# Kernel tuning notes

Measured on AMD Instinct MI355X. Metric: run time of the kernel, lower is better.

## Reference

```python
import jax, jax.numpy as jnp
import numpy as np

NEGPOS_RATIO = 3


def _smooth_l1(pred, tgt):
    d = jnp.abs(pred - tgt)
    return jnp.where(d < 1.0, 0.5 * d * d, d - 0.5)


def setup_inputs() -> dict:
    key = jax.random.key(0)
    B, P, C = 64, 8732, 81
    ks = jax.random.split(key, 7)
    loc_dataT = jax.random.normal(ks[0], (B, P, 4), jnp.float32)
    conf_dataT = jax.random.normal(ks[1], (B, P, C), jnp.float32)
    loc_dataS = jax.random.normal(ks[2], (B, P, 4), jnp.float32)
    conf_dataS = jax.random.normal(ks[3], (B, P, C), jnp.float32)
    loc_t = jax.random.normal(ks[4], (B, P, 4), jnp.float32)
    is_pos = jax.random.uniform(ks[5], (B, P)) < 0.02
    labels = jax.random.randint(ks[6], (B, P), 1, C, dtype=jnp.int32)
    conf_t = jnp.where(is_pos, labels, 0).astype(jnp.int32)
    return {
        "loc_dataT": loc_dataT, "conf_dataT": conf_dataT,
        "loc_dataS": loc_dataS, "conf_dataS": conf_dataS,
        "loc_t": loc_t, "conf_t": conf_t,
    }


def _multibox_losses(loc_dataT, conf_dataT, loc_dataS, conf_dataS, loc_t, conf_t):
    B, P, C = conf_dataT.shape
    pos = conf_t > 0                                    # [B,P]
    posf = pos.astype(conf_dataT.dtype)

    # Localization SmoothL1 over positive priors (reduction='sum')
    loss_lT = jnp.sum(_smooth_l1(loc_dataT, loc_t) * posf[..., None])
    loss_lS = jnp.sum(_smooth_l1(loc_dataS, loc_t) * posf[..., None])

    # Per-prior CE loss: logsumexp(conf) - conf[gt]  (== -log_softmax[gt])
    def per_prior_ce(conf):
        lse = jax.nn.logsumexp(conf, axis=-1)           # [B,P]
        gt = jnp.take_along_axis(conf, conf_t[..., None].astype(jnp.int32), axis=-1)[..., 0]
        return lse - gt

    lcT = per_prior_ce(conf_dataT)                      # [B,P]
    lcS = per_prior_ce(conf_dataS)

    # Hard negative mining: rank negatives by loss (positives zeroed first)
    def neg_mask(lc, num_neg):
        lc_m = jnp.where(pos, 0.0, lc)
        order = jnp.argsort(-lc_m, axis=1)              # descending sort indices
        rank = jnp.argsort(order, axis=1)               # rank of each prior
        return rank < num_neg

    num_pos = jnp.sum(pos.astype(jnp.int32), axis=1, keepdims=True)   # [B,1]
    num_neg = jnp.minimum(NEGPOS_RATIO * num_pos, P - 1)
    negT = neg_mask(lcT, num_neg)
    negS = neg_mask(lcS, num_neg)

    # Confidence CE over positives + mined negatives (reduction='sum')
    loss_cT = jnp.sum(jnp.where(pos | negT, lcT, 0.0))
    loss_cS = jnp.sum(jnp.where(pos | negS, lcS, 0.0))

    N = jnp.sum(num_pos).astype(conf_dataT.dtype)
    return jnp.stack([loss_lT / N, loss_cT / N, loss_lS / N, loss_cS / N])


def reference(loc_dataT, conf_dataT, loc_dataS, conf_dataS, loc_t, conf_t):
    # Teacher branch is detached in the original module.
    loc_dataT = jax.lax.stop_gradient(loc_dataT)
    conf_dataT = jax.lax.stop_gradient(conf_dataT)
    return _multibox_losses(loc_dataT, conf_dataT, loc_dataS, conf_dataS, loc_t, conf_t)
```

## Files before the change

kernel.cpp:

```cpp
#include <hip/hip_runtime.h>
#include <hip/hip_bf16.h>

#define BB 64
#define PP 8732
#define CC 81
#define RPB 128


__device__ __forceinline__ float sl1(float d) {
    d = fabsf(d);
    return d < 1.0f ? 0.5f * d * d : d - 0.5f;
}

__device__ __forceinline__ float blockReduceF(float v, volatile float* sb) {
    for (int off = 32; off; off >>= 1) v += __shfl_xor(v, off, 64);
    __syncthreads();
    if ((threadIdx.x & 63) == 0) sb[threadIdx.x >> 6] = v;
    __syncthreads();
    float r = 0.0f;
    int nw = blockDim.x >> 6;
    for (int i = 0; i < nw; ++i) r += sb[i];
    return r;
}

__device__ __forceinline__ int blockReduceI(int v, volatile int* sb) {
    for (int off = 32; off; off >>= 1) v += __shfl_xor(v, off, 64);
    __syncthreads();
    if ((threadIdx.x & 63) == 0) sb[threadIdx.x >> 6] = v;
    __syncthreads();
    int r = 0;
    int nw = blockDim.x >> 6;
    for (int i = 0; i < nw; ++i) r += sb[i];
    return r;
}

__global__ void kInit(float* acc, int* numpos) {
    int t = threadIdx.x;
    if (t < 4) acc[t] = 0.0f;
    if (t < BB) numpos[t] = 0;
}

__global__ __launch_bounds__(1024) void kA(const float4* __restrict__ locT,
                                           const float4* __restrict__ locS,
                                           const float4* __restrict__ loct,
                                           const int* __restrict__ conft,
                                           float* acc, int* numpos) {
    __shared__ float fsb[16];
    __shared__ int isb[16];
    int b = blockIdx.y;
    int p = blockIdx.x * blockDim.x + threadIdx.x;
    float sT = 0.0f, sS = 0.0f;
    int cnt = 0;
    if (p < PP) {
        size_t i = (size_t)b * PP + p;
        int t = conft[i];
        if (t > 0) {
            cnt = 1;
            float4 g = loct[i];
            float4 aT = locT[i];
            float4 aS = locS[i];
            sT = sl1(aT.x - g.x) + sl1(aT.y - g.y) + sl1(aT.z - g.z) + sl1(aT.w - g.w);
            sS = sl1(aS.x - g.x) + sl1(aS.y - g.y) + sl1(aS.z - g.z) + sl1(aS.w - g.w);
        }
    }
    sT = blockReduceF(sT, fsb);
    sS = blockReduceF(sS, fsb);
    cnt = blockReduceI(cnt, isb);
    if (threadIdx.x == 0) {
        if (sT != 0.0f) atomicAdd(&acc[0], sT);
        if (sS != 0.0f) atomicAdd(&acc[1], sS);
        if (cnt) atomicAdd(&numpos[b], cnt);
    }
}

__global__ __launch_bounds__(256) void kB(const float* __restrict__ confT,
                                          const float* __restrict__ confS,
                                          const int* __restrict__ conft,
                                          float* __restrict__ lcT,
                                          float* __restrict__ lcS) {
    __shared__ float rowsum[RPB];
    __shared__ float gtval[RPB];
    __shared__ int gtofs[RPB];
    __shared__ int gtraw[RPB];
    int b = blockIdx.y;
    int p0 = blockIdx.x * RPB;
    int nrows = min(RPB, PP - p0);
    int tid = threadIdx.x;
    const float* __restrict__ conf = blockIdx.z ? confS : confT;
    float* __restrict__ dst = blockIdx.z ? lcS : lcT;
    size_t rowBase = (size_t)b * PP + p0;

    for (int r = tid; r < nrows; r += 256) {
        int g = conft[rowBase + r];
        gtraw[r] = g;
        gtofs[r] = r * CC + g;
        rowsum[r] = 0.0f;
        gtval[r] = 0.0f;
    }
    __syncthreads();

    const float4* __restrict__ g4 = (const float4*)(conf + rowBase * CC);
    int nq = (nrows * CC) >> 2;
    for (int i = tid; i < nq; i += 256) {
        float4 v = g4[i];
        int f = i << 2;
        int r0 = f / 81;
        int rem = f - r0 * 81;
        int r1 = (rem + 3 >= 81) ? r0 + 1 : r0;
        float e0 = __expf(v.x), e1 = __expf(v.y), e2 = __expf(v.z), e3 = __expf(v.w);
        float t01 = e0 + e1, t23 = e2 + e3, tot = t01 + t23;
        if (r1 == r0) {
            atomicAdd(&rowsum[r0], tot);
        } else {
            int nsplit = 81 - rem;
            float a = (nsplit == 1) ? e0 : ((nsplit == 2) ? t01 : t01 + e2);
            atomicAdd(&rowsum[r0], a);
            atomicAdd(&rowsum[r1], tot - a);
        }
        int j = gtofs[r0] - f;
        if (j >= 0 && j < 4) gtval[r0] = ((const float*)&v)[j];
        if (r1 != r0) {
            int j1 = gtofs[r1] - f;
            if (j1 >= 0 && j1 < 4) gtval[r1] = ((const float*)&v)[j1];
        }
    }
    __syncthreads();

    for (int r = tid; r < nrows; r += 256) {
        float lc = __logf(rowsum[r]) - gtval[r];
        dst[rowBase + r] = (gtraw[r] > 0) ? -(lc + 1.0f) : lc;
    }
}

__global__ __launch_bounds__(1024) void kC(const float* __restrict__ lcT,
                                           const float* __restrict__ lcS,
                                           const int* __restrict__ numpos,
                                           float* acc) {
    __shared__ unsigned keys[PP];
    __shared__ int hist[256];
    __shared__ float fsb[16];
    __shared__ int isb[16];
    __shared__ int selBin, selAbove;
    int b = blockIdx.y;
    int tid = threadIdx.x;
    const float* src = ((blockIdx.x == 0) ? lcT : lcS) + (size_t)b * PP;

    float posSum = 0.0f;
    for (int i = tid; i < PP; i += 1024) {
        float v = src[i];
        keys[i] = (v < 0.0f) ? 0u : __float_as_uint(v);
        if (v < 0.0f) posSum += (-v - 1.0f);
    }
    posSum = blockReduceF(posSum, fsb);

    int np = numpos[b];
    int k = min(3 * np, PP - 1);
    float mined = 0.0f;
    if (k > 0) {
        unsigned prefix = 0;
        int kk = k;
        for (int round = 0; round < 4; ++round) {
            int shift = 24 - 8 * round;
            if (tid < 256) hist[tid] = 0;
            __syncthreads();
            for (int i = tid; i < PP; i += 1024) {
                unsigned key = keys[i];
                bool match = (round == 0) || ((key >> (shift + 8)) == prefix);
                if (match) atomicAdd(&hist[(key >> shift) & 0xFF], 1);
            }
            __syncthreads();
            for (int d = 1; d < 256; d <<= 1) {
                int v2 = 0;
                if (tid < 256) v2 = hist[tid] + ((tid + d < 256) ? hist[tid + d] : 0);
                __syncthreads();
                if (tid < 256) hist[tid] = v2;
                __syncthreads();
            }
            if (tid < 256) {
                int above = (tid < 255) ? hist[tid + 1] : 0;
                if (above < kk && hist[tid] >= kk) {
                    selBin = tid;
                    selAbove = above;
                }
            }
            __syncthreads();
            prefix = (prefix << 8) | (unsigned)selBin;
            kk -= selAbove;
            __syncthreads();
        }
        int c = 0;
        float s = 0.0f;
        for (int i = tid; i < PP; i += 1024) {
            unsigned key = keys[i];
            if (key > prefix) { c += 1; s += __uint_as_float(key); }
        }
        c = blockReduceI(c, isb);
        s = blockReduceF(s, fsb);
        mined = s + (float)(k - c) * __uint_as_float(prefix);
    }
    if (tid == 0) atomicAdd(&acc[(blockIdx.x == 0) ? 2 : 3], posSum + mined);
}

__global__ void kD(const float* acc, const int* numpos, float* out) {
    int v = (threadIdx.x < BB) ? numpos[threadIdx.x] : 0;
    for (int off = 32; off; off >>= 1) v += __shfl_xor(v, off, 64);
    if (threadIdx.x == 0) {
        float N = (float)v;
        out[0] = acc[0] / N;
        out[1] = acc[2] / N;
        out[2] = acc[1] / N;
        out[3] = acc[3] / N;
    }
}

extern "C" void kernel_launch(void* const* d_in, const int* in_sizes, int n_in,
                              void* d_out, int out_size, void* d_ws, size_t ws_size,
                              hipStream_t stream) {
    const float* locT  = (const float*)d_in[0];
    const float* confT = (const float*)d_in[1];
    const float* locS  = (const float*)d_in[2];
    const float* confS = (const float*)d_in[3];
    const float* loct  = (const float*)d_in[4];
    const int*   conft = (const int*)d_in[5];
    float* out = (float*)d_out;

    float* lcT = (float*)d_ws;
    float* lcS = lcT + (size_t)BB * PP;
    float* acc = lcS + (size_t)BB * PP;
    int* numpos = (int*)(acc + 4);

    kInit<<<1, 64, 0, stream>>>(acc, numpos);

    dim3 gA((PP + 1023) / 1024, BB);
    kA<<<gA, 1024, 0, stream>>>((const float4*)locT, (const float4*)locS,
                                (const float4*)loct, conft, acc, numpos);

    dim3 gB((PP + RPB - 1) / RPB, BB, 2);
    kB<<<gB, 256, 0, stream>>>(confT, confS, conft, lcT, lcS);

    dim3 gC(2, BB);
    kC<<<gC, 1024, 0, stream>>>(lcT, lcS, numpos, acc);

    kD<<<1, 64, 0, stream>>>(acc, numpos, out);
}
```

Baseline: 509.2 us.

## Replace shared-memory atomics in row logsumexp with per-slot partial sums

The softmax-CE kernel no longer accumulates each row's exp-sum with shared-memory atomicAdd. Each float4 slot now writes its partial sum to a shared array, with a separate spill array for the part of a slot that crosses into the next row. Two threads per row then sum the slots and combine with a shuffle. Full tiles issue all eleven float4 loads up front before computing, to get more memory-level parallelism. The cost is about 10 KB more shared memory per block and higher register use from the unrolled loads.

Measured after the change: 424.8 us. 16.6% less time.

```diff
diff --git a/kernel.cpp b/kernel.cpp
--- a/kernel.cpp
+++ b/kernel.cpp
@@ -5,6 +5,7 @@
 #define PP 8732
 #define CC 81
 #define RPB 128
+#define SLOTS ((RPB * CC) / 4)
 
 
 __device__ __forceinline__ float sl1(float d) {
@@ -73,12 +74,39 @@
     }
 }
 
+__device__ __forceinline__ void processSlot(int i, float4 v,
+                                            float* psum, float* spill,
+                                            const int* gtofs, float* gtval) {
+    int f = i << 2;
+    int r0 = f / 81;
+    int rem = f - r0 * 81;
+    float e0 = __expf(v.x), e1 = __expf(v.y), e2 = __expf(v.z), e3 = __expf(v.w);
+    float t01 = e0 + e1;
+    float tot = t01 + e2 + e3;
+    float ps = tot;
+    bool split = rem >= 78;
+    if (split) {
+        int ns = 81 - rem;
+        float a = (ns == 1) ? e0 : ((ns == 2) ? t01 : t01 + e2);
+        ps = a;
+        spill[r0 + 1] = tot - a;
+    }
+    psum[i] = ps;
+    int j = gtofs[r0] - f;
+    if (j >= 0 && j < 4) gtval[r0] = ((const float*)&v)[j];
+    if (split) {
+        int j1 = gtofs[r0 + 1] - f;
+        if (j1 >= 0 && j1 < 4) gtval[r0 + 1] = ((const float*)&v)[j1];
+    }
+}
+
 __global__ __launch_bounds__(256) void kB(const float* __restrict__ confT,
                                           const float* __restrict__ confS,
                                           const int* __restrict__ conft,
                                           float* __restrict__ lcT,
                                           float* __restrict__ lcS) {
-    __shared__ float rowsum[RPB];
+    __shared__ float psum[SLOTS];
+    __shared__ float spill[RPB];
     __shared__ float gtval[RPB];
     __shared__ int gtofs[RPB];
     __shared__ int gtraw[RPB];
@@ -90,45 +118,49 @@
     float* __restrict__ dst = blockIdx.z ? lcS : lcT;
     size_t rowBase = (size_t)b * PP + p0;
 
-    for (int r = tid; r < nrows; r += 256) {
-        int g = conft[rowBase + r];
-        gtraw[r] = g;
-        gtofs[r] = r * CC + g;
-        rowsum[r] = 0.0f;
-        gtval[r] = 0.0f;
+    if (tid < nrows) {
+        int g = conft[rowBase + tid];
+        gtraw[tid] = g;
+        gtofs[tid] = tid * CC + g;
+        spill[tid] = 0.0f;
+        gtval[tid] = 0.0f;
     }
     __syncthreads();
 
     const float4* __restrict__ g4 = (const float4*)(conf + rowBase * CC);
     int nq = (nrows * CC) >> 2;
-    for (int i = tid; i < nq; i += 256) {
-        float4 v = g4[i];
-        int f = i << 2;
-        int r0 = f / 81;
-        int rem = f - r0 * 81;
-        int r1 = (rem + 3 >= 81) ? r0 + 1 : r0;
-        float e0 = __expf(v.x), e1 = __expf(v.y), e2 = __expf(v.z), e3 = __expf(v.w);
-        float t01 = e0 + e1, t23 = e2 + e3, tot = t01 + t23;
-        if (r1 == r0) {
-            atomicAdd(&rowsum[r0], tot);
-        } else {
-            int nsplit = 81 - rem;
-            float a = (nsplit == 1) ? e0 : ((nsplit == 2) ? t01 : t01 + e2);
-            atomicAdd(&rowsum[r0], a);
-            atomicAdd(&rowsum[r1], tot - a);
-        }
-        int j = gtofs[r0] - f;
-        if (j >= 0 && j < 4) gtval[r0] = ((const float*)&v)[j];
-        if (r1 != r0) {
-            int j1 = gtofs[r1] - f;
-            if (j1 >= 0 && j1 < 4) gtval[r1] = ((const float*)&v)[j1];
-        }
-    }
-    __syncthreads();
-
-    for (int r = tid; r < nrows; r += 256) {
-        float lc = __logf(rowsum[r]) - gtval[r];
-        dst[rowBase + r] = (gtraw[r] > 0) ? -(lc + 1.0f) : lc;
+
+    if (nrows == RPB) {
+        float4 v[10];
+        #pragma unroll
+        for (int k = 0; k < 10; ++k) v[k] = g4[tid + 256 * k];
+        float4 vx;
+        bool extra = tid < (SLOTS - 2560);
+        if (extra) vx = g4[2560 + tid];
+        #pragma unroll
+        for (int k = 0; k < 10; ++k)
+            processSlot(tid + 256 * k, v[k], psum, spill, gtofs, gtval);
+        if (extra) processSlot(2560 + tid, vx, psum, spill, gtofs, gtval);
+    } else {
+        for (int i = tid; i < nq; i += 256)
+            processSlot(i, g4[i], psum, spill, gtofs, gtval);
+    }
+    __syncthreads();
+
+    int r = tid >> 1, h = tid & 1;
+    if (r < nrows) {
+        int i0 = (81 * r + 3) >> 2;
+        int i1 = (81 * (r + 1) + 3) >> 2;
+        int mid = (i0 + i1 + 1) >> 1;
+        int lo = h ? mid : i0;
+        int hi = h ? i1 : mid;
+        float s = h ? 0.0f : spill[r];
+        for (int i = lo; i < hi; ++i) s += psum[i];
+        s += __shfl_xor(s, 1, 64);
+        if (h == 0) {
+            float lc = __logf(s) - gtval[r];
+            dst[rowBase + r] = (gtraw[r] > 0) ? -(lc + 1.0f) : lc;
+        }
     }
 }
 
```
